# Performance work log

Measured on AMD Instinct MI355X. Metric: run time of the kernel, lower is better.

The kernel has to match this reference:

```python
import jax, jax.numpy as jnp
import numpy as np


def _l2norm(x, eps=1e-6):
    # Matches F.normalize(p=2, dim=-1, eps=eps): divide by max(||x||, eps)
    n = jnp.sqrt(jnp.sum(x * x, axis=-1, keepdims=True))
    return x / jnp.maximum(n, eps)


def setup_inputs() -> dict:
    key = jax.random.key(0)
    k0, k1, k2, k3, k4 = jax.random.split(key, 5)
    B, T, H, Dk, Dv = 2, 4096, 16, 128, 128
    q = _l2norm(jax.random.normal(k0, (B, T, H, Dk), dtype=jnp.float32))
    k = _l2norm(jax.random.normal(k1, (B, T, H, Dk), dtype=jnp.float32))
    v = jax.random.normal(k2, (B, T, H, Dv), dtype=jnp.float32)
    # alpha: decay in (0,1) (module: exp(-exp(A_log)*softplus(a+dt_bias)))
    alpha = jax.random.uniform(k3, (B, T, H), dtype=jnp.float32, minval=0.5, maxval=0.999)
    # beta: write gate in (0,1) (module: sigmoid(b))
    beta = jax.random.uniform(k4, (B, T, H), dtype=jnp.float32, minval=0.01, maxval=0.99)
    initial_state = jnp.zeros((B, H, Dk, Dv), dtype=jnp.float32)
    return {"q": q, "k": k, "v": v, "alpha": alpha, "beta": beta,
            "initial_state": initial_state}


def reference(q, k, v, alpha, beta, initial_state):
    """Gated delta rule recurrence (faithful to gdn_recurrent_naive).

    S_t = a_t * (S_{t-1} - b_t * k_t (k_t^T S_{t-1})) + b_t * k_t v_t^T
    o_t = S_t^T q_t
    """
    def step(S, xs):
        q_t, k_t, v_t, a_t, b_t = xs  # (B,H,Dk), (B,H,Dk), (B,H,Dv), (B,H), (B,H)
        a = a_t[..., None, None]
        b = b_t[..., None, None]
        kS = jnp.einsum('bhd,bhdv->bhv', k_t, S)          # k^T S
        S = a * (S - b * jnp.einsum('bhd,bhv->bhdv', k_t, kS)) \
            + b * jnp.einsum('bhd,bhv->bhdv', k_t, v_t)   # delta-rule update
        o = jnp.einsum('bhdv,bhd->bhv', S, q_t)           # read with q
        return S, o

    xs = (q.swapaxes(0, 1), k.swapaxes(0, 1), v.swapaxes(0, 1),
          alpha.swapaxes(0, 1), beta.swapaxes(0, 1))  # time-major for scan
    S_final, outs = jax.lax.scan(step, initial_state.astype(jnp.float32), xs)
    return outs.swapaxes(0, 1), S_final  # (B,T,H,Dv), (B,H,Dk,Dv)
```

## Files before the change

### kernel.cpp

```cpp
#include <hip/hip_runtime.h>

#define T_LEN 4096
#define H_N   16
#define DK    128
#define DV    128
#define LCH   64
#define NCH   64

typedef float f32x4 __attribute__((ext_vector_type(4)));
typedef short s16x8 __attribute__((ext_vector_type(8)));

#define OFF_U0 0
#define OFF_W  32768
#define OFF_Q  49152
#define OFF_KD 65536
#define OFF_G  81920
#define OFF_GM 90112
#define CH_B   90368ull
#define WS_NEED (2048ull * CH_B)

#define SWZ(row) (((row)&7) << 4)

#define AST 68
#define RST 132

__device__ __forceinline__ unsigned short f2b(float x) {
  unsigned u = __float_as_uint(x);
  return (unsigned short)((u + 0x7FFF + ((u >> 16) & 1)) >> 16);
}

#define GLDS16(gp, lp)                                                        \
  __builtin_amdgcn_global_load_lds(                                           \
      (const __attribute__((address_space(1))) void*)(gp),                    \
      (__attribute__((address_space(3))) void*)(lp), 16, 0, 0)
#define GLDS4(gp, lp)                                                         \
  __builtin_amdgcn_global_load_lds(                                           \
      (const __attribute__((address_space(1))) void*)(gp),                    \
      (__attribute__((address_space(3))) void*)(lp), 4, 0, 0)

#define LBAR()                                                                \
  do {                                                                        \
    asm volatile("s_waitcnt lgkmcnt(0)" ::: "memory");                        \
    __builtin_amdgcn_s_barrier();                                             \
    __builtin_amdgcn_sched_barrier(0);                                        \
  } while (0)

__device__ void solve64(float* RHS, const float* A, int tid) {
#pragma unroll 1
  for (int I = 0; I < 4; ++I) {
    if (I > 0) {
      const int i2 = 16 * I + (tid >> 4), cg = tid & 15;
      float* rp = RHS + i2 * RST + cg * 8;
      f32x4 a0 = *(const f32x4*)(rp);
      f32x4 a1 = *(const f32x4*)(rp + 4);
      for (int j = 0; j < 16 * I; ++j) {
        float a = A[i2 * AST + j];
        const float* yp = RHS + j * RST + cg * 8;
        f32x4 y0 = *(const f32x4*)(yp);
        f32x4 y1 = *(const f32x4*)(yp + 4);
#pragma unroll
        for (int e = 0; e < 4; ++e) {
          a0[e] = fmaf(-a, y0[e], a0[e]);
          a1[e] = fmaf(-a, y1[e], a1[e]);
        }
      }
      *(f32x4*)(rp) = a0;
      *(f32x4*)(rp + 4) = a1;
      __syncthreads();
    }
    if (tid < 128) {
      const int col = tid;
      float y[16];
#pragma unroll
      for (int r = 0; r < 16; ++r) y[r] = RHS[(16 * I + r) * RST + col];
#pragma unroll
      for (int r = 1; r < 16; ++r) {
        float t0 = 0.f, t1 = 0.f;
#pragma unroll
        for (int j = 0; j < 15; ++j)
          if (j < r) {
            float av = A[(16 * I + r) * AST + 16 * I + j];
            if (j & 1) t1 = fmaf(av, y[j], t1);
            else       t0 = fmaf(av, y[j], t0);
          }
        y[r] -= t0 + t1;
      }
#pragma unroll
      for (int r = 0; r < 16; ++r) RHS[(16 * I + r) * RST + col] = y[r];
    }
    __syncthreads();
  }
}

extern "C" __global__ void __launch_bounds__(256) gdn_p1(
    const float* __restrict__ q, const float* __restrict__ k,
    const float* __restrict__ v, const float* __restrict__ al,
    const float* __restrict__ be, char* __restrict__ ws) {
  __shared__ __align__(16) unsigned char big[34048];
  __shared__ __align__(16) float A_s[64 * AST];
  __shared__ float g_s[64], bb_s[64], sc_s[64];
  unsigned char* Kb = big;
  unsigned char* Qb = big + 16384;
  float* RHS = (float*)big;

  const int bid = blockIdx.x;
  const int bh = bid & 31, c = bid >> 5;
  const int b = bh >> 4, h = bh & 15;
  const int tid = threadIdx.x;
  const int t0 = c * LCH;
  char* wsc = ws + (size_t)(bh * 64 + c) * CH_B;

  if (tid < 64) {
    size_t gi = (size_t)(b * T_LEN + t0 + tid) * H_N + h;
    float x = __logf(al[gi]);
    bb_s[tid] = be[gi];
#pragma unroll
    for (int d = 1; d < 64; d <<= 1) {
      float yv = __shfl_up(x, d, 64);
      if (tid >= d) x += yv;
    }
    float gam = __expf(x);
    g_s[tid] = x;
    sc_s[tid] = gam;
    *(float*)(wsc + OFF_GM + tid * 4) = gam;
  }

  for (int idx = tid; idx < 1024; idx += 256) {
    int row = idx >> 4, grp = idx & 15;
    size_t go = ((size_t)(b * T_LEN + t0 + row) * H_N + h) * DK + grp * 8;
    float4 ka = *(const float4*)(k + go);
    float4 kb2 = *(const float4*)(k + go + 4);
    float4 qa = *(const float4*)(q + go);
    float4 qb2 = *(const float4*)(q + go + 4);
    union { unsigned short u[8]; uint4 v4; } tk, tq;
    tk.u[0] = f2b(ka.x); tk.u[1] = f2b(ka.y); tk.u[2] = f2b(ka.z); tk.u[3] = f2b(ka.w);
    tk.u[4] = f2b(kb2.x); tk.u[5] = f2b(kb2.y); tk.u[6] = f2b(kb2.z); tk.u[7] = f2b(kb2.w);
    tq.u[0] = f2b(qa.x); tq.u[1] = f2b(qa.y); tq.u[2] = f2b(qa.z); tq.u[3] = f2b(qa.w);
    tq.u[4] = f2b(qb2.x); tq.u[5] = f2b(qb2.y); tq.u[6] = f2b(qb2.z); tq.u[7] = f2b(qb2.w);
    int la = (row * 256 + grp * 16) ^ SWZ(row);
    *(uint4*)(Kb + la) = tk.v4;
    *(uint4*)(Qb + la) = tq.v4;
    *(uint4*)(wsc + OFF_Q + la) = tq.v4;
  }
  __syncthreads();

  const int w = tid >> 6, l = tid & 63, li = l & 15, hi = l >> 4;
  f32x4 aK[4], aQ[4];
#pragma unroll
  for (int jt = 0; jt < 4; ++jt) { aK[jt] = (f32x4){0, 0, 0, 0}; aQ[jt] = (f32x4){0, 0, 0, 0}; }
#pragma unroll
  for (int ks = 0; ks < 4; ++ks) {
    int rowA = 16 * w + li;
    int oa = (rowA * 256 + ks * 64 + hi * 16) ^ SWZ(rowA);
    s16x8 fa = *(const s16x8*)(Kb + oa);
    s16x8 fq = *(const s16x8*)(Qb + oa);
#pragma unroll
    for (int jt = 0; jt < 4; ++jt) {
      int rowB = 16 * jt + li;
      s16x8 fb = *(const s16x8*)(Kb + ((rowB * 256 + ks * 64 + hi * 16) ^ SWZ(rowB)));
      aK[jt] = __builtin_amdgcn_mfma_f32_16x16x32_bf16(fa, fb, aK[jt], 0, 0, 0);
      aQ[jt] = __builtin_amdgcn_mfma_f32_16x16x32_bf16(fq, fb, aQ[jt], 0, 0, 0);
    }
  }
#pragma unroll
  for (int jt = 0; jt < 4; ++jt)
#pragma unroll
    for (int r = 0; r < 4; ++r) {
      int i = 16 * w + hi * 4 + r, j = 16 * jt + li;
      float e = __expf(g_s[i] - g_s[j]);
      A_s[i * AST + j] = (j < i) ? bb_s[i] * e * aK[jt][r] : 0.f;
      *(unsigned short*)(wsc + OFF_G + ((i * 128 + j * 2) ^ SWZ(i))) =
          f2b((j <= i) ? e * aQ[jt][r] : 0.f);
    }
  __syncthreads();

  for (int idx = tid; idx < 2048; idx += 256) {
    int row = idx >> 5, c4 = idx & 31;
    float4 vv = *(const float4*)(v + ((size_t)(b * T_LEN + t0 + row) * H_N + h) * DV + c4 * 4);
    float s = bb_s[row];
    float4 o = {s * vv.x, s * vv.y, s * vv.z, s * vv.w};
    *(float4*)(RHS + row * RST + c4 * 4) = o;
  }
  __syncthreads();
  solve64(RHS, A_s, tid);
  for (int idx = tid; idx < 2048; idx += 256) {
    int row = idx >> 5, c4 = idx & 31;
    *(float4*)(wsc + OFF_U0 + (c4 >> 2) * 4096 + row * 64 + (c4 & 3) * 16) =
        *(const float4*)(RHS + row * RST + c4 * 4);
  }
  __syncthreads();

  for (int idx = tid; idx < 2048; idx += 256) {
    int row = idx >> 5, c4 = idx & 31;
    float4 kv = *(const float4*)(k + ((size_t)(b * T_LEN + t0 + row) * H_N + h) * DK + c4 * 4);
    float s = bb_s[row] * sc_s[row];
    float4 o = {s * kv.x, s * kv.y, s * kv.z, s * kv.w};
    *(float4*)(RHS + row * RST + c4 * 4) = o;
  }
  __syncthreads();
  solve64(RHS, A_s, tid);
  for (int idx = tid; idx < 1024; idx += 256) {
    int row = idx >> 4, g8 = idx & 15;
    const float* p = RHS + row * RST + g8 * 8;
    union { unsigned short u[8]; uint4 v4; } t;
#pragma unroll
    for (int e = 0; e < 8; ++e) t.u[e] = f2b(-p[e]);
    *(uint4*)(wsc + OFF_W + ((row * 256 + g8 * 16) ^ SWZ(row))) = t.v4;
  }
  __syncthreads();

  if (tid < 64) sc_s[tid] = __expf(g_s[63] - g_s[tid]);
  __syncthreads();
  float* Kf = (float*)big;
#pragma unroll 1
  for (int p = 0; p < 2; ++p) {
    for (int idx = tid; idx < 1024; idx += 256) {
      int r = idx >> 5, c4 = idx & 31;
      float4 kv = *(const float4*)(k + ((size_t)(b * T_LEN + t0 + 32 * p + r) * H_N + h) * DK + c4 * 4);
      *(float4*)(Kf + r * 132 + c4 * 4) = kv;
    }
    __syncthreads();
#pragma unroll
    for (int m = 0; m < 16; ++m) {
      int flat = m * 256 + tid;
      int j32 = flat & 31, d = flat >> 5;
      float val = sc_s[32 * p + j32] * Kf[j32 * 132 + d];
      *(unsigned short*)(wsc + OFF_KD + ((d * 128 + (32 * p + j32) * 2) ^ SWZ(d))) = f2b(val);
    }
    __syncthreads();
  }
}

extern "C" __global__ void __launch_bounds__(256, 1) gdn_p2(
    const float* __restrict__ S0, float* __restrict__ out,
    const char* __restrict__ ws) {
  __shared__ unsigned char Wb[2][16384];
  __shared__ unsigned char Qb[2][16384];
  __shared__ unsigned char KDb[2][16384];
  __shared__ unsigned char Gb[2][8192];
  __shared__ float U0s[2][1024];
  __shared__ float gam[2][64];
  __shared__ unsigned char Stb[4096];
  __shared__ unsigned char Ytb[2048];

  const int bid = blockIdx.x;
  const int bh = bid & 31, s = bid >> 5;
  const int b = bh >> 4, h = bh & 15;
  const int tid = threadIdx.x;
  const int w = tid >> 6, lane = tid & 63, li = lane & 15, hi = lane >> 4;
  const char* wsbase = ws + (size_t)bh * 64 * CH_B;

#define STG(CI, P)                                                            \
  do {                                                                        \
    const char* c_ = wsbase + (size_t)(CI) * CH_B;                            \
    _Pragma("unroll") for (int j_ = 0; j_ < 4; ++j_) {                        \
      GLDS16(c_ + OFF_W + j_ * 4096 + tid * 16, &Wb[P][j_ * 4096 + w * 1024]); \
      GLDS16(c_ + OFF_Q + j_ * 4096 + tid * 16, &Qb[P][j_ * 4096 + w * 1024]); \
      GLDS16(c_ + OFF_KD + j_ * 4096 + tid * 16, &KDb[P][j_ * 4096 + w * 1024]); \
    }                                                                         \
    _Pragma("unroll") for (int j_ = 0; j_ < 2; ++j_)                          \
      GLDS16(c_ + OFF_G + j_ * 4096 + tid * 16, &Gb[P][j_ * 4096 + w * 1024]); \
    GLDS16(c_ + OFF_U0 + s * 4096 + tid * 16,                                 \
           (unsigned char*)U0s[P] + w * 1024);                                \
    if (w == 0) GLDS4(c_ + OFF_GM + lane * 4, &gam[P][0]);                    \
  } while (0)

  float S[2][4];
#pragma unroll
  for (int t = 0; t < 2; ++t)
#pragma unroll
    for (int r = 0; r < 4; ++r) {
      int d = (w + 4 * t) * 16 + hi * 4 + r;
      S[t][r] = S0[((size_t)bh * 128 + d) * 128 + s * 16 + li];
    }
#define WRITE_ST()                                                            \
  do {                                                                        \
    _Pragma("unroll") for (int t = 0; t < 2; ++t)                             \
        _Pragma("unroll") for (int r = 0; r < 4; r += 2) {                    \
      int d = (w + 4 * t) * 16 + hi * 4 + r;                                  \
      unsigned pk = (unsigned)f2b(S[t][r]) | ((unsigned)f2b(S[t][r + 1]) << 16); \
      *(unsigned*)(Stb + ((li * 256 + d * 2) ^ SWZ(li))) = pk;                \
    }                                                                         \
  } while (0)

  STG(0, 0);
  WRITE_ST();
  __syncthreads();

#pragma unroll 1
  for (int c = 0; c < NCH; ++c) {
    const int p = c & 1;
    if (c + 1 < NCH) STG(c + 1, p ^ 1);

    s16x8 sfb[4];
#pragma unroll
    for (int ks = 0; ks < 4; ++ks)
      sfb[ks] = *(const s16x8*)(Stb + ((li * 256 + ks * 64 + hi * 16) ^ SWZ(li)));

    f32x4 Y;
#pragma unroll
    for (int r = 0; r < 4; ++r) Y[r] = U0s[p][(16 * w + hi * 4 + r) * 16 + li];
#pragma unroll
    for (int ks = 0; ks < 4; ++ks) {
      s16x8 fa = *(const s16x8*)(Wb[p] + (((16 * w + li) * 256 + ks * 64 + hi * 16) ^ SWZ(li)));
      Y = __builtin_amdgcn_mfma_f32_16x16x32_bf16(fa, sfb[ks], Y, 0, 0, 0);
    }
#pragma unroll
    for (int r = 0; r < 4; r += 2) {
      int j = 16 * w + hi * 4 + r;
      unsigned pk = (unsigned)f2b(Y[r]) | ((unsigned)f2b(Y[r + 1]) << 16);
      *(unsigned*)(Ytb + ((li * 128 + j * 2) ^ SWZ(li))) = pk;
    }
    LBAR();

    f32x4 O = {0, 0, 0, 0};
#pragma unroll
    for (int ks = 0; ks < 4; ++ks) {
      s16x8 fa = *(const s16x8*)(Qb[p] + (((16 * w + li) * 256 + ks * 64 + hi * 16) ^ SWZ(li)));
      O = __builtin_amdgcn_mfma_f32_16x16x32_bf16(fa, sfb[ks], O, 0, 0, 0);
    }
    s16x8 yfb[2];
#pragma unroll
    for (int ks = 0; ks < 2; ++ks)
      yfb[ks] = *(const s16x8*)(Ytb + ((li * 128 + ks * 64 + hi * 16) ^ SWZ(li)));
#pragma unroll
    for (int r = 0; r < 4; ++r) O[r] *= gam[p][16 * w + hi * 4 + r];
#pragma unroll
    for (int ks = 0; ks < 2; ++ks) {
      s16x8 fa = *(const s16x8*)(Gb[p] + (((16 * w + li) * 128 + ks * 64 + hi * 16) ^ SWZ(li)));
      O = __builtin_amdgcn_mfma_f32_16x16x32_bf16(fa, yfb[ks], O, 0, 0, 0);
    }
#pragma unroll
    for (int r = 0; r < 4; ++r) {
      size_t oi = ((size_t)(b * T_LEN + c * 64 + 16 * w + hi * 4 + r) * H_N + h) * DV + s * 16 + li;
      out[oi] = O[r];
    }

    float ge = gam[p][63];
#pragma unroll
    for (int t = 0; t < 2; ++t) {
      f32x4 acc;
#pragma unroll
      for (int r = 0; r < 4; ++r) acc[r] = ge * S[t][r];
#pragma unroll
      for (int ks = 0; ks < 2; ++ks) {
        s16x8 fa = *(const s16x8*)(KDb[p] + ((((w + 4 * t) * 16 + li) * 128 + ks * 64 + hi * 16) ^ SWZ(li)));
        acc = __builtin_amdgcn_mfma_f32_16x16x32_bf16(fa, yfb[ks], acc, 0, 0, 0);
      }
#pragma unroll
      for (int r = 0; r < 4; ++r) S[t][r] = acc[r];
    }
    LBAR();
    WRITE_ST();
    __syncthreads();
  }

#pragma unroll
  for (int t = 0; t < 2; ++t)
#pragma unroll
    for (int r = 0; r < 4; ++r) {
      int d = (w + 4 * t) * 16 + hi * 4 + r;
      out[(size_t)(2 * T_LEN * H_N * DV) + ((size_t)bh * 128 + d) * 128 + s * 16 + li] = S[t][r];
    }
}

#define COLS 16
#define CHUNK 16
#define STEP_B 8192u
#define AB_B 64u
#define OSTRIDE (H_N * DV)
template <int CTRL>
__device__ __forceinline__ float dpp_add(float x) {
  int y = __builtin_amdgcn_update_dpp(0, __float_as_int(x), CTRL, 0xF, 0xF, true);
  return x + __int_as_float(y);
}
__device__ __forceinline__ float red16(float x) {
  x = dpp_add<0xB1>(x); x = dpp_add<0x4E>(x);
  x = dpp_add<0x124>(x); x = dpp_add<0x128>(x);
  return x;
}
extern "C" __global__ void __launch_bounds__(256, 1) gdn_fallback(
    const float* __restrict__ q, const float* __restrict__ k,
    const float* __restrict__ v, const float* __restrict__ al,
    const float* __restrict__ be, const float* __restrict__ S0,
    float* __restrict__ out) {
  __shared__ float kb[2][CHUNK * DK];
  __shared__ float qb[2][CHUNK * DK];
  __shared__ float vb[2][CHUNK * COLS];
  __shared__ float abuf[2][64];
  __shared__ float bbuf[2][64];
  const int bid = blockIdx.x;
  const int bh = bid & 31, g = bid >> 5;
  const int b = bh >> 4, h = bh & 15;
  const int tid = threadIdx.x;
  const int cl = tid >> 4, li = tid & 15, lane = tid & 63, wid = tid >> 6;
  const int col = g * COLS + cl, d0 = li * 8;
  const size_t bh_qk = ((size_t)b * T_LEN * H_N + h) * DK;
  const size_t bh_v = ((size_t)b * T_LEN * H_N + h) * DV;
  const size_t bh_ab = (size_t)b * T_LEN * H_N + h;
  const int fo0 = wid * 2048 + lane * 16, fo1 = fo0 + 1024;
  const char* kg0 = (const char*)(k + bh_qk) + (size_t)(fo0 >> 9) * STEP_B + (fo0 & 511);
  const char* kg1 = (const char*)(k + bh_qk) + (size_t)(fo1 >> 9) * STEP_B + (fo1 & 511);
  const char* qg0 = (const char*)(q + bh_qk) + (size_t)(fo0 >> 9) * STEP_B + (fo0 & 511);
  const char* qg1 = (const char*)(q + bh_qk) + (size_t)(fo1 >> 9) * STEP_B + (fo1 & 511);
  const int fv = lane * 16;
  const char* vg = (const char*)(v + bh_v + g * COLS) + (size_t)(fv >> 6) * STEP_B + (fv & 63);
  const int lcl = lane < 16 ? lane : 15;
  const char* ag = (const char*)(al + bh_ab) + (size_t)lcl * AB_B;
  const char* bg = (const char*)(be + bh_ab) + (size_t)lcl * AB_B;
#define STAGEF(CI, P) do { \
    const size_t off = (size_t)(CI) * (CHUNK * STEP_B); \
    const size_t offab = (size_t)(CI) * (CHUNK * AB_B); \
    GLDS16(kg0 + off, &kb[P][wid * 512]); GLDS16(kg1 + off, &kb[P][wid * 512 + 256]); \
    GLDS16(qg0 + off, &qb[P][wid * 512]); GLDS16(qg1 + off, &qb[P][wid * 512 + 256]); \
    if (wid == 0) GLDS16(vg + off, &vb[P][0]); \
    else if (wid == 1) GLDS4(ag + offab, &abuf[P][0]); \
    else if (wid == 2) GLDS4(bg + offab, &bbuf[P][0]); \
  } while (0)
  float sv[8];
  const float* s0p = S0 + ((size_t)(b * H_N + h) * DK + d0) * DV + col;
#pragma unroll
  for (int j = 0; j < 8; ++j) sv[j] = s0p[(size_t)j * DV];
  STAGEF(0, 0);
  __syncthreads();
  float* op = out + bh_v + col;
  for (int ci = 0; ci < T_LEN / CHUNK; ++ci) {
    const int p = ci & 1;
    if (ci + 1 < T_LEN / CHUNK) STAGEF(ci + 1, p ^ 1);
    const float* kc = kb[p]; const float* qc = qb[p]; const float* vc = vb[p];
    const float* ac = abuf[p]; const float* bc = bbuf[p];
#pragma unroll
    for (int j = 0; j < CHUNK; ++j) {
      f32x4 kA = *(const f32x4*)(kc + j * DK + d0);
      f32x4 kB = *(const f32x4*)(kc + j * DK + d0 + 4);
      f32x4 qA = *(const f32x4*)(qc + j * DK + d0);
      f32x4 qB = *(const f32x4*)(qc + j * DK + d0 + 4);
      float vv = vc[j * COLS + cl], aa = ac[j], bv = bc[j];
      float kk[8] = {kA[0], kA[1], kA[2], kA[3], kB[0], kB[1], kB[2], kB[3]};
      float qq[8] = {qA[0], qA[1], qA[2], qA[3], qB[0], qB[1], qB[2], qB[3]};
      float pk0 = kk[0] * sv[0], pk1 = kk[1] * sv[1];
      float pu0 = qq[0] * sv[0], pu1 = qq[1] * sv[1];
      float pg0 = kk[0] * qq[0], pg1 = kk[1] * qq[1];
#pragma unroll
      for (int m = 2; m < 8; m += 2) {
        pk0 = fmaf(kk[m], sv[m], pk0); pk1 = fmaf(kk[m + 1], sv[m + 1], pk1);
        pu0 = fmaf(qq[m], sv[m], pu0); pu1 = fmaf(qq[m + 1], sv[m + 1], pu1);
        pg0 = fmaf(kk[m], qq[m], pg0); pg1 = fmaf(kk[m + 1], qq[m + 1], pg1);
      }
      float pk = red16(pk0 + pk1), pu = red16(pu0 + pu1), pg = red16(pg0 + pg1);
      float tmp = fmaf(-(bv * aa), pk, bv * vv);
#pragma unroll
      for (int m = 0; m < 8; ++m) sv[m] = fmaf(aa, sv[m], kk[m] * tmp);
      if (li == 0) op[(size_t)(ci * CHUNK + j) * OSTRIDE] = fmaf(pg, tmp, aa * pu);
    }
    __syncthreads();
  }
  float* sf = out + (size_t)2 * T_LEN * H_N * DV + ((size_t)(b * H_N + h) * DK + d0) * DV + col;
#pragma unroll
  for (int j = 0; j < 8; ++j) sf[(size_t)j * DV] = sv[j];
}

extern "C" void kernel_launch(void* const* d_in, const int* in_sizes, int n_in,
                              void* d_out, int out_size, void* d_ws,
                              size_t ws_size, hipStream_t stream) {
  const float* q = (const float*)d_in[0];
  const float* k = (const float*)d_in[1];
  const float* v = (const float*)d_in[2];
  const float* al = (const float*)d_in[3];
  const float* be = (const float*)d_in[4];
  const float* S0 = (const float*)d_in[5];
  float* out = (float*)d_out;

  if (ws_size >= WS_NEED) {
    gdn_p1<<<dim3(2048), dim3(256), 0, stream>>>(q, k, v, al, be, (char*)d_ws);
    gdn_p2<<<dim3(256), dim3(256), 0, stream>>>(S0, out, (const char*)d_ws);
  } else {
    gdn_fallback<<<dim3(256), dim3(256), 0, stream>>>(q, k, v, al, be, S0, out);
  }
}
```

Baseline: 294.3 us.

## Split chunk recurrence across two warp groups to shorten the serial critical path

Doubles the p2 block to 512 threads and specialises the two halves. Group A computes Y = U0 + W·S and the intra-chunk output correction. Group B computes the Q·S inter-chunk output, passes it through shared memory, and performs the state update and state write-back. This aims to cut per-chunk serial latency in the sequential 64-chunk loop by overlapping independent MFMA chains. In exchange it adds an extra shared buffer, one more LDS round-trip for the partial output, and twice the wave count per block.

```diff
diff --git a/kernel.cpp b/kernel.cpp
--- a/kernel.cpp
+++ b/kernel.cpp
@@ -231,7 +231,7 @@
   }
 }
 
-extern "C" __global__ void __launch_bounds__(256, 1) gdn_p2(
+extern "C" __global__ void __launch_bounds__(512, 1) gdn_p2(
     const float* __restrict__ S0, float* __restrict__ out,
     const char* __restrict__ ws) {
   __shared__ unsigned char Wb[2][16384];
@@ -242,49 +242,54 @@
   __shared__ float gam[2][64];
   __shared__ unsigned char Stb[4096];
   __shared__ unsigned char Ytb[2048];
+  __shared__ float Oa[1024];
 
   const int bid = blockIdx.x;
   const int bh = bid & 31, s = bid >> 5;
   const int b = bh >> 4, h = bh & 15;
   const int tid = threadIdx.x;
-  const int w = tid >> 6, lane = tid & 63, li = lane & 15, hi = lane >> 4;
+  const int w = tid >> 6;
+  const int lane = tid & 63, li = lane & 15, hi = lane >> 4;
+  const int wq = w & 3;
+  const bool grpA = (w < 4);
   const char* wsbase = ws + (size_t)bh * 64 * CH_B;
 
 #define STG(CI, P)                                                            \
   do {                                                                        \
     const char* c_ = wsbase + (size_t)(CI) * CH_B;                            \
-    _Pragma("unroll") for (int j_ = 0; j_ < 4; ++j_) {                        \
-      GLDS16(c_ + OFF_W + j_ * 4096 + tid * 16, &Wb[P][j_ * 4096 + w * 1024]); \
-      GLDS16(c_ + OFF_Q + j_ * 4096 + tid * 16, &Qb[P][j_ * 4096 + w * 1024]); \
-      GLDS16(c_ + OFF_KD + j_ * 4096 + tid * 16, &KDb[P][j_ * 4096 + w * 1024]); \
+    _Pragma("unroll") for (int j_ = 0; j_ < 2; ++j_) {                        \
+      GLDS16(c_ + OFF_W + j_ * 8192 + tid * 16, &Wb[P][j_ * 8192 + w * 1024]); \
+      GLDS16(c_ + OFF_Q + j_ * 8192 + tid * 16, &Qb[P][j_ * 8192 + w * 1024]); \
+      GLDS16(c_ + OFF_KD + j_ * 8192 + tid * 16, &KDb[P][j_ * 8192 + w * 1024]); \
     }                                                                         \
-    _Pragma("unroll") for (int j_ = 0; j_ < 2; ++j_)                          \
-      GLDS16(c_ + OFF_G + j_ * 4096 + tid * 16, &Gb[P][j_ * 4096 + w * 1024]); \
-    GLDS16(c_ + OFF_U0 + s * 4096 + tid * 16,                                 \
-           (unsigned char*)U0s[P] + w * 1024);                                \
-    if (w == 0) GLDS4(c_ + OFF_GM + lane * 4, &gam[P][0]);                    \
+    GLDS16(c_ + OFF_G + tid * 16, &Gb[P][w * 1024]);                          \
+    if (w < 4) GLDS16(c_ + OFF_U0 + s * 4096 + tid * 16,                      \
+                      (unsigned char*)U0s[P] + w * 1024);                     \
+    if (w == 7) GLDS4(c_ + OFF_GM + lane * 4, &gam[P][0]);                    \
   } while (0)
 
   float S[2][4];
-#pragma unroll
-  for (int t = 0; t < 2; ++t)
-#pragma unroll
-    for (int r = 0; r < 4; ++r) {
-      int d = (w + 4 * t) * 16 + hi * 4 + r;
-      S[t][r] = S0[((size_t)bh * 128 + d) * 128 + s * 16 + li];
-    }
+  if (!grpA) {
+#pragma unroll
+    for (int t = 0; t < 2; ++t)
+#pragma unroll
+      for (int r = 0; r < 4; ++r) {
+        int d = (wq + 4 * t) * 16 + hi * 4 + r;
+        S[t][r] = S0[((size_t)bh * 128 + d) * 128 + s * 16 + li];
+      }
+  }
 #define WRITE_ST()                                                            \
   do {                                                                        \
     _Pragma("unroll") for (int t = 0; t < 2; ++t)                             \
         _Pragma("unroll") for (int r = 0; r < 4; r += 2) {                    \
-      int d = (w + 4 * t) * 16 + hi * 4 + r;                                  \
+      int d = (wq + 4 * t) * 16 + hi * 4 + r;                                 \
       unsigned pk = (unsigned)f2b(S[t][r]) | ((unsigned)f2b(S[t][r + 1]) << 16); \
       *(unsigned*)(Stb + ((li * 256 + d * 2) ^ SWZ(li))) = pk;                \
     }                                                                         \
   } while (0)
 
   STG(0, 0);
-  WRITE_ST();
+  if (!grpA) WRITE_ST();
   __syncthreads();
 
 #pragma unroll 1
@@ -297,71 +302,84 @@
     for (int ks = 0; ks < 4; ++ks)
       sfb[ks] = *(const s16x8*)(Stb + ((li * 256 + ks * 64 + hi * 16) ^ SWZ(li)));
 
-    f32x4 Y;
-#pragma unroll
-    for (int r = 0; r < 4; ++r) Y[r] = U0s[p][(16 * w + hi * 4 + r) * 16 + li];
-#pragma unroll
-    for (int ks = 0; ks < 4; ++ks) {
-      s16x8 fa = *(const s16x8*)(Wb[p] + (((16 * w + li) * 256 + ks * 64 + hi * 16) ^ SWZ(li)));
-      Y = __builtin_amdgcn_mfma_f32_16x16x32_bf16(fa, sfb[ks], Y, 0, 0, 0);
-    }
-#pragma unroll
-    for (int r = 0; r < 4; r += 2) {
-      int j = 16 * w + hi * 4 + r;
-      unsigned pk = (unsigned)f2b(Y[r]) | ((unsigned)f2b(Y[r + 1]) << 16);
-      *(unsigned*)(Ytb + ((li * 128 + j * 2) ^ SWZ(li))) = pk;
-    }
-    LBAR();
-
-    f32x4 O = {0, 0, 0, 0};
-#pragma unroll
-    for (int ks = 0; ks < 4; ++ks) {
-      s16x8 fa = *(const s16x8*)(Qb[p] + (((16 * w + li) * 256 + ks * 64 + hi * 16) ^ SWZ(li)));
-      O = __builtin_amdgcn_mfma_f32_16x16x32_bf16(fa, sfb[ks], O, 0, 0, 0);
-    }
-    s16x8 yfb[2];
-#pragma unroll
-    for (int ks = 0; ks < 2; ++ks)
-      yfb[ks] = *(const s16x8*)(Ytb + ((li * 128 + ks * 64 + hi * 16) ^ SWZ(li)));
-#pragma unroll
-    for (int r = 0; r < 4; ++r) O[r] *= gam[p][16 * w + hi * 4 + r];
-#pragma unroll
-    for (int ks = 0; ks < 2; ++ks) {
-      s16x8 fa = *(const s16x8*)(Gb[p] + (((16 * w + li) * 128 + ks * 64 + hi * 16) ^ SWZ(li)));
-      O = __builtin_amdgcn_mfma_f32_16x16x32_bf16(fa, yfb[ks], O, 0, 0, 0);
-    }
-#pragma unroll
-    for (int r = 0; r < 4; ++r) {
-      size_t oi = ((size_t)(b * T_LEN + c * 64 + 16 * w + hi * 4 + r) * H_N + h) * DV + s * 16 + li;
-      out[oi] = O[r];
-    }
-
-    float ge = gam[p][63];
-#pragma unroll
-    for (int t = 0; t < 2; ++t) {
-      f32x4 acc;
-#pragma unroll
-      for (int r = 0; r < 4; ++r) acc[r] = ge * S[t][r];
+    if (grpA) {
+      f32x4 Y;
+#pragma unroll
+      for (int r = 0; r < 4; ++r) Y[r] = U0s[p][(16 * wq + hi * 4 + r) * 16 + li];
+#pragma unroll
+      for (int ks = 0; ks < 4; ++ks) {
+        s16x8 fa = *(const s16x8*)(Wb[p] + (((16 * wq + li) * 256 + ks * 64 + hi * 16) ^ SWZ(li)));
+        Y = __builtin_amdgcn_mfma_f32_16x16x32_bf16(fa, sfb[ks], Y, 0, 0, 0);
+      }
+#pragma unroll
+      for (int r = 0; r < 4; r += 2) {
+        int j = 16 * wq + hi * 4 + r;
+        unsigned pk = (unsigned)f2b(Y[r]) | ((unsigned)f2b(Y[r + 1]) << 16);
+        *(unsigned*)(Ytb + ((li * 128 + j * 2) ^ SWZ(li))) = pk;
+      }
+      LBAR();
+      f32x4 O;
+      s16x8 yfb[2];
+#pragma unroll
+      for (int ks = 0; ks < 2; ++ks)
+        yfb[ks] = *(const s16x8*)(Ytb + ((li * 128 + ks * 64 + hi * 16) ^ SWZ(li)));
+#pragma unroll
+      for (int r = 0; r < 4; ++r) O[r] = Oa[(16 * wq + hi * 4 + r) * 16 + li];
 #pragma unroll
       for (int ks = 0; ks < 2; ++ks) {
-        s16x8 fa = *(const s16x8*)(KDb[p] + ((((w + 4 * t) * 16 + li) * 128 + ks * 64 + hi * 16) ^ SWZ(li)));
-        acc = __builtin_amdgcn_mfma_f32_16x16x32_bf16(fa, yfb[ks], acc, 0, 0, 0);
-      }
-#pragma unroll
-      for (int r = 0; r < 4; ++r) S[t][r] = acc[r];
-    }
-    LBAR();
-    WRITE_ST();
+        s16x8 fa = *(const s16x8*)(Gb[p] + (((16 * wq + li) * 128 + ks * 64 + hi * 16) ^ SWZ(li)));
+        O = __builtin_amdgcn_mfma_f32_16x16x32_bf16(fa, yfb[ks], O, 0, 0, 0);
+      }
+#pragma unroll
+      for (int r = 0; r < 4; ++r) {
+        size_t oi = ((size_t)(b * T_LEN + c * 64 + 16 * wq + hi * 4 + r) * H_N + h) * DV + s * 16 + li;
+        out[oi] = O[r];
+      }
+    } else {
+      f32x4 Oq = {0, 0, 0, 0};
+#pragma unroll
+      for (int ks = 0; ks < 4; ++ks) {
+        s16x8 fa = *(const s16x8*)(Qb[p] + (((16 * wq + li) * 256 + ks * 64 + hi * 16) ^ SWZ(li)));
+        Oq = __builtin_amdgcn_mfma_f32_16x16x32_bf16(fa, sfb[ks], Oq, 0, 0, 0);
+      }
+#pragma unroll
+      for (int r = 0; r < 4; ++r) {
+        int row = 16 * wq + hi * 4 + r;
+        Oa[row * 16 + li] = gam[p][row] * Oq[r];
+      }
+      LBAR();
+      s16x8 yfb[2];
+#pragma unroll
+      for (int ks = 0; ks < 2; ++ks)
+        yfb[ks] = *(const s16x8*)(Ytb + ((li * 128 + ks * 64 + hi * 16) ^ SWZ(li)));
+      float ge = gam[p][63];
+#pragma unroll
+      for (int t = 0; t < 2; ++t) {
+        f32x4 acc;
+#pragma unroll
+        for (int r = 0; r < 4; ++r) acc[r] = ge * S[t][r];
+#pragma unroll
+        for (int ks = 0; ks < 2; ++ks) {
+          s16x8 fa = *(const s16x8*)(KDb[p] + ((((wq + 4 * t) * 16 + li) * 128 + ks * 64 + hi * 16) ^ SWZ(li)));
+          acc = __builtin_amdgcn_mfma_f32_16x16x32_bf16(fa, yfb[ks], acc, 0, 0, 0);
+        }
+#pragma unroll
+        for (int r = 0; r < 4; ++r) S[t][r] = acc[r];
+      }
+      WRITE_ST();
+    }
     __syncthreads();
   }
 
-#pragma unroll
-  for (int t = 0; t < 2; ++t)
-#pragma unroll
-    for (int r = 0; r < 4; ++r) {
-      int d = (w + 4 * t) * 16 + hi * 4 + r;
-      out[(size_t)(2 * T_LEN * H_N * DV) + ((size_t)bh * 128 + d) * 128 + s * 16 + li] = S[t][r];
-    }
+  if (!grpA) {
+#pragma unroll
+    for (int t = 0; t < 2; ++t)
+#pragma unroll
+      for (int r = 0; r < 4; ++r) {
+        int d = (wq + 4 * t) * 16 + hi * 4 + r;
+        out[(size_t)(2 * T_LEN * H_N * DV) + ((size_t)bh * 128 + d) * 128 + s * 16 + li] = S[t][r];
+      }
+  }
 }
 
 #define COLS 16
@@ -473,7 +491,7 @@
 
   if (ws_size >= WS_NEED) {
     gdn_p1<<<dim3(2048), dim3(256), 0, stream>>>(q, k, v, al, be, (char*)d_ws);
-    gdn_p2<<<dim3(256), dim3(256), 0, stream>>>(S0, out, (const char*)d_ws);
+    gdn_p2<<<dim3(256), dim3(512), 0, stream>>>(S0, out, (const char*)d_ws);
   } else {
     gdn_fallback<<<dim3(256), dim3(256), 0, stream>>>(q, k, v, al, be, S0, out);
   }
```

New measurement: 282.0 us. 4.2% less time.
